# Optimization experiments

Measured on AMD Instinct MI355X. Metric: run time of the kernel, lower is better.

Reference implementation:

```python
import jax, jax.numpy as jnp
import numpy as np
from math import sqrt

H = 16
D_MODEL = 1024
D_K = D_MODEL // H
B, S = 2, 2048


def setup_inputs() -> dict:
    key = jax.random.key(0)
    ks = jax.random.split(key, 12)
    scale = 1.0 / sqrt(D_MODEL)
    inp = {
        "query": jax.random.normal(ks[0], (B, S, D_MODEL), jnp.float32),
        "key": jax.random.normal(ks[1], (B, S, D_MODEL), jnp.float32),
        "value": jax.random.normal(ks[2], (B, S, D_MODEL), jnp.float32),
        # causal mask [B, S, S]; module unsqueezes head dim itself
        "mask": jnp.broadcast_to(jnp.tril(jnp.ones((S, S), jnp.int32)), (B, S, S)),
        "Wq": jax.random.normal(ks[3], (D_MODEL, D_MODEL), jnp.float32) * scale,
        "bq": jnp.zeros((D_MODEL,), jnp.float32),
        "Wk": jax.random.normal(ks[4], (D_MODEL, D_MODEL), jnp.float32) * scale,
        "bk": jnp.zeros((D_MODEL,), jnp.float32),
        "Wv": jax.random.normal(ks[5], (D_MODEL, D_MODEL), jnp.float32) * scale,
        "bv": jnp.zeros((D_MODEL,), jnp.float32),
        "Wo": jax.random.normal(ks[6], (D_MODEL, D_MODEL), jnp.float32) * scale,
        "bo": jnp.zeros((D_MODEL,), jnp.float32),
    }
    return inp


def reference(query, key, value, mask, Wq, bq, Wk, bk, Wv, bv, Wo, bo):
    nb = query.shape[0]

    def proj(x, W, b):
        # nn.Linear: x @ W.T + b, then split heads -> [B, H, S, D_K]
        y = jnp.einsum('bsd,ed->bse', x, W) + b
        return y.reshape(nb, -1, H, D_K).transpose(0, 2, 1, 3)

    q = proj(query, Wq, bq)
    k = proj(key, Wk, bk)
    v = proj(value, Wv, bv)

    scores = jnp.einsum('bhqd,bhkd->bhqk', q, k) / sqrt(D_K)  # [B,H,S,S]
    scores = jnp.where(mask[:, None, :, :] == 0, -jnp.inf, scores)
    probs = jax.nn.softmax(scores, axis=-1)  # dropout in eval mode (identity)
    ctx = jnp.einsum('bhqk,bhkd->bhqd', probs, v)
    ctx = ctx.transpose(0, 2, 1, 3).reshape(nb, -1, H * D_K)
    return jnp.einsum('bsd,ed->bse', ctx, Wo) + bo
```

## Files before the change

### kernel.cpp

```cpp
#include <hip/hip_runtime.h>
#include <hip/hip_bf16.h>
#include <stdint.h>


#define H_ 16
#define DM 1024
#define DK_ 64
#define BB 2
#define SS 2048
#define PSTR 72

typedef __bf16 bf16x8 __attribute__((ext_vector_type(8)));
typedef __bf16 bf16x2_t __attribute__((ext_vector_type(2)));
typedef float f32x4 __attribute__((ext_vector_type(4)));

#define GLOAD_LDS16(g, l)                                            \
  __builtin_amdgcn_global_load_lds(                                  \
      (__attribute__((address_space(1))) void*)(g),                  \
      (__attribute__((address_space(3))) void*)(l), 16, 0, 0)

__device__ __forceinline__ unsigned short f2bf_u(float f) {
  unsigned int u = __float_as_uint(f);
  u += 0x7fffu + ((u >> 16) & 1u);
  return (unsigned short)(u >> 16);
}

__device__ __forceinline__ unsigned int pack_bf16(float a, float b) {
#if __has_builtin(__builtin_amdgcn_cvt_pk_bf16_f32)
  bf16x2_t v = __builtin_amdgcn_cvt_pk_bf16_f32(a, b);
  unsigned int u;
  __builtin_memcpy(&u, &v, 4);
  return u;
#else
  return (unsigned int)f2bf_u(a) | ((unsigned int)f2bf_u(b) << 16);
#endif
}

__device__ __forceinline__ float fexp2(float x) {
#if __has_builtin(__builtin_amdgcn_exp2f)
  return __builtin_amdgcn_exp2f(x);
#else
  return exp2f(x);
#endif
}

struct Cvt {
  const float* s[7];
  unsigned short* d[7];
  int n[7];
};

__global__ __launch_bounds__(256) void convert_kernel(Cvt c) {
  const int y = blockIdx.y;
  const float* __restrict__ src = c.s[y];
  unsigned short* __restrict__ dst = c.d[y];
  const int nv = c.n[y] >> 2;
  for (int i = blockIdx.x * 256 + threadIdx.x; i < nv; i += 1024 * 256) {
    float4 v = *(const float4*)(src + (size_t)i * 4);
    ushort4 o;
    o.x = f2bf_u(v.x); o.y = f2bf_u(v.y); o.z = f2bf_u(v.z); o.w = f2bf_u(v.w);
    *(ushort4*)(dst + (size_t)i * 4) = o;
  }
}

template <int TN>
__device__ __forceinline__ void gemm_dbuf(
    const unsigned short* __restrict__ A, const unsigned short* __restrict__ W,
    unsigned short* As, unsigned short* Bs, int m0, int n0,
    f32x4 (*acc)[TN / 32]) {
  constexpr int FW = TN / 32;
  const int tid = threadIdx.x;
  const int wave = tid >> 6, lane = tid & 63;
  const int lm = lane & 15, quad = lane >> 4;
  const int wm = (wave >> 1) * 64, wn = (wave & 1) * (16 * FW);
  const int srow = lane >> 2;
  const int scol = (lane & 3) * 8;

#pragma unroll
  for (int i = 0; i < 4; ++i)
#pragma unroll
    for (int j = 0; j < FW; ++j) {
      f32x4 z = {0.f, 0.f, 0.f, 0.f};
      acc[i][j] = z;
    }

#pragma unroll
  for (int cc = 0; cc < 2; ++cc) {
    int c = wave * 2 + cc;
    GLOAD_LDS16(A + (size_t)(m0 + c * 16 + srow) * DM + scol,
                As + c * 512 + lane * 8);
  }
  if (TN == 128) {
#pragma unroll
    for (int cc = 0; cc < 2; ++cc) {
      int c = wave * 2 + cc;
      GLOAD_LDS16(W + (size_t)(n0 + c * 16 + srow) * DM + scol,
                  Bs + c * 512 + lane * 8);
    }
  } else {
    GLOAD_LDS16(W + (size_t)(n0 + wave * 16 + srow) * DM + scol,
                Bs + wave * 512 + lane * 8);
  }

  for (int kt = 0; kt < DM / 32; ++kt) {
    __syncthreads();
    const int cur = kt & 1;
    const unsigned short* Ac = As + cur * (128 * 32);
    const unsigned short* Bc = Bs + cur * (TN * 32);
    if (kt + 1 < DM / 32) {
      unsigned short* An = As + (cur ^ 1) * (128 * 32);
      unsigned short* Bn = Bs + (cur ^ 1) * (TN * 32);
      const int kcol = (kt + 1) * 32 + scol;
#pragma unroll
      for (int cc = 0; cc < 2; ++cc) {
        int c = wave * 2 + cc;
        GLOAD_LDS16(A + (size_t)(m0 + c * 16 + srow) * DM + kcol,
                    An + c * 512 + lane * 8);
      }
      if (TN == 128) {
#pragma unroll
        for (int cc = 0; cc < 2; ++cc) {
          int c = wave * 2 + cc;
          GLOAD_LDS16(W + (size_t)(n0 + c * 16 + srow) * DM + kcol,
                      Bn + c * 512 + lane * 8);
        }
      } else {
        GLOAD_LDS16(W + (size_t)(n0 + wave * 16 + srow) * DM + kcol,
                    Bn + wave * 512 + lane * 8);
      }
    }
    bf16x8 af[4], bfr[FW];
#pragma unroll
    for (int i = 0; i < 4; ++i)
      af[i] = *(const bf16x8*)(Ac + (wm + i * 16 + lm) * 32 + quad * 8);
#pragma unroll
    for (int j = 0; j < FW; ++j)
      bfr[j] = *(const bf16x8*)(Bc + (wn + j * 16 + lm) * 32 + quad * 8);
#pragma unroll
    for (int i = 0; i < 4; ++i)
#pragma unroll
      for (int j = 0; j < FW; ++j)
        acc[i][j] = __builtin_amdgcn_mfma_f32_16x16x32_bf16(af[i], bfr[j],
                                                            acc[i][j], 0, 0, 0);
  }
}

__global__ __launch_bounds__(512, 2) void qkv_gemm(
    const unsigned short* Qi, const unsigned short* Ki, const unsigned short* Vi,
    const unsigned short* Wq, const unsigned short* Wk, const unsigned short* Wv,
    const float* bq, const float* bk, const float* bv,
    unsigned short* Qf, unsigned short* Kf, unsigned short* Vf) {
  __shared__ unsigned short As[2 * 2 * 16 * 512];
  __shared__ unsigned short Bs[2 * 2 * 16 * 512];
  const int p = blockIdx.x;
  const int c = p & 7, idx = p >> 3;
  const int x = idx & 3, yy = (idx >> 2) & 1, z = idx >> 3;
  const int y = c * 2 + yy;
  const int m0 = y * 256, n0 = x * 256;
  const unsigned short* A = z == 0 ? Qi : (z == 1 ? Ki : Vi);
  const unsigned short* W = z == 0 ? Wq : (z == 1 ? Wk : Wv);
  const float* bias = z == 0 ? bq : (z == 1 ? bk : bv);
  const float scale = z == 0 ? 0.1803368801111204f : 1.0f;

  const int tid = threadIdx.x;
  const int wave = tid >> 6, lane = tid & 63;
  const int lm = lane & 15, quad = lane >> 4;
  const int wr = wave >> 2, wc = wave & 3;

  const int scs = 8 * ((lane & 3) ^ ((lane >> 3) & 3));
  const size_t asrc0 = (size_t)(m0 + wave * 16 + (lane >> 2)) * DM + scs;
  const size_t bsrc0 = (size_t)(n0 + wave * 16 + (lane >> 2)) * DM + scs;
  const int sdst = wave * 512 + lane * 8;

  const int rcol = (quad * 8) ^ (((lm >> 1) & 3) * 8);
  const int aoff = wr * 8 * 512 + lm * 32 + rcol;
  const int boff = wc * 4 * 512 + lm * 32 + rcol;

  f32x4 acc[8][4];
#pragma unroll
  for (int i = 0; i < 8; ++i)
#pragma unroll
    for (int j = 0; j < 4; ++j) {
      f32x4 zz = {0.f, 0.f, 0.f, 0.f};
      acc[i][j] = zz;
    }

  auto stA = [&](int buf, int kh, int kt) {
    const unsigned short* s = A + asrc0 + (size_t)kt * 64 + kh * 32;
    unsigned short* d = As + buf * 16384 + kh * 8192 + sdst;
    GLOAD_LDS16(s, d);
    GLOAD_LDS16(s + (size_t)128 * DM, d + 4096);
  };
  auto stB = [&](int buf, int kh, int kt) {
    const unsigned short* s = W + bsrc0 + (size_t)kt * 64 + kh * 32;
    unsigned short* d = Bs + buf * 16384 + kh * 8192 + sdst;
    GLOAD_LDS16(s, d);
    GLOAD_LDS16(s + (size_t)128 * DM, d + 4096);
  };

  stA(0, 0, 0); stB(0, 0, 0); stA(0, 1, 0); stB(0, 1, 0);
  stA(1, 0, 1); stB(1, 0, 1); stA(1, 1, 1);
  asm volatile("s_waitcnt vmcnt(6)" ::: "memory");
  __builtin_amdgcn_s_barrier();

#define BARR __builtin_amdgcn_s_barrier()
#define SCHB __builtin_amdgcn_sched_barrier(0)
#define MFMA8(AF, B0_, B1_, J0, J1)                                          \
  __builtin_amdgcn_s_setprio(1);                                             \
  _Pragma("unroll")                                                          \
  for (int i = 0; i < 8; ++i) {                                              \
    acc[i][J0] = __builtin_amdgcn_mfma_f32_16x16x32_bf16(AF[i], B0_,         \
                                                         acc[i][J0], 0, 0, 0); \
    acc[i][J1] = __builtin_amdgcn_mfma_f32_16x16x32_bf16(AF[i], B1_,         \
                                                         acc[i][J1], 0, 0, 0); \
  }                                                                          \
  __builtin_amdgcn_s_setprio(0)

#pragma unroll 2
  for (int t = 0; t < 14; ++t) {
    const int buf = t & 1;
    const unsigned short* Ab = As + buf * 16384;
    const unsigned short* Bb = Bs + buf * 16384;
    bf16x8 a0[8], b0[4];
#pragma unroll
    for (int i = 0; i < 8; ++i)
      a0[i] = *(const bf16x8*)(Ab + aoff + i * 512);
#pragma unroll
    for (int j = 0; j < 4; ++j)
      b0[j] = *(const bf16x8*)(Bb + boff + j * 512);
    stB(buf ^ 1, 1, t + 1);
    BARR; SCHB;
    MFMA8(a0, b0[0], b0[1], 0, 1);
    SCHB; BARR;
    stA(buf, 0, t + 2);
    BARR; SCHB;
    MFMA8(a0, b0[2], b0[3], 2, 3);
    SCHB; BARR;
    bf16x8 a1[8], b1[4];
#pragma unroll
    for (int i = 0; i < 8; ++i)
      a1[i] = *(const bf16x8*)(Ab + 8192 + aoff + i * 512);
#pragma unroll
    for (int j = 0; j < 4; ++j)
      b1[j] = *(const bf16x8*)(Bb + 8192 + boff + j * 512);
    stB(buf, 0, t + 2);
    BARR; SCHB;
    MFMA8(a1, b1[0], b1[1], 0, 1);
    SCHB; BARR;
    stA(buf, 1, t + 2);
    asm volatile("s_waitcnt vmcnt(6)" ::: "memory");
    BARR; SCHB;
    MFMA8(a1, b1[2], b1[3], 2, 3);
    SCHB; BARR;
  }

  stB(1, 1, 15);
  asm volatile("s_waitcnt vmcnt(0)" ::: "memory");
  __builtin_amdgcn_s_barrier();
#pragma unroll
  for (int tt = 0; tt < 2; ++tt) {
    const unsigned short* Ab = As + tt * 16384;
    const unsigned short* Bb = Bs + tt * 16384;
#pragma unroll
    for (int kh = 0; kh < 2; ++kh) {
      bf16x8 a2[8], b2[4];
#pragma unroll
      for (int i = 0; i < 8; ++i)
        a2[i] = *(const bf16x8*)(Ab + kh * 8192 + aoff + i * 512);
#pragma unroll
      for (int j = 0; j < 4; ++j)
        b2[j] = *(const bf16x8*)(Bb + kh * 8192 + boff + j * 512);
#pragma unroll
      for (int i = 0; i < 8; ++i)
#pragma unroll
        for (int j = 0; j < 4; ++j)
          acc[i][j] = __builtin_amdgcn_mfma_f32_16x16x32_bf16(
              a2[i], b2[j], acc[i][j], 0, 0, 0);
    }
  }
#undef MFMA8
#undef SCHB
#undef BARR

  if (z == 2) {
#pragma unroll
    for (int j = 0; j < 4; ++j) {
      int gn = n0 + wc * 64 + j * 16 + lm;
      float bv_ = bias[gn];
      int h2 = gn >> 6, dk = gn & 63;
      int a = dk >> 4, ln = dk & 15;
#pragma unroll
      for (int i = 0; i < 8; ++i) {
        int s0 = m0 + wr * 128 + i * 16 + quad * 4;
        int b2 = s0 >> 11, sl = s0 & 2047;
        int kt2 = sl >> 6, cc2 = (sl >> 5) & 1, qk = (sl >> 3) & 3, j0 = sl & 7;
        size_t base =
            ((size_t)(((b2 * 16 + h2) * 32 + kt2) * 4 + a) * 2 + cc2) * 512 +
            (qk * 16 + ln) * 8 + j0;
        uint2 w;
        w.x = pack_bf16(acc[i][j][0] + bv_, acc[i][j][1] + bv_);
        w.y = pack_bf16(acc[i][j][2] + bv_, acc[i][j][3] + bv_);
        *(uint2*)(Vf + base) = w;
      }
    }
  } else {
    unsigned short* out = z == 0 ? Qf : Kf;
#pragma unroll
    for (int j = 0; j < 4; ++j) {
      int gn = n0 + wc * 64 + j * 16 + lm;
      float bv_ = bias[gn];
      int h2 = gn >> 6, d64 = gn & 63;
      int cc2 = (d64 >> 5) & 1, qk = (d64 >> 3) & 3, jjq = d64 & 7;
#pragma unroll
      for (int i = 0; i < 8; ++i)
#pragma unroll
        for (int r = 0; r < 4; ++r) {
          int gm = m0 + wr * 128 + i * 16 + quad * 4 + r;
          int b2 = gm >> 11, sl = gm & 2047;
          size_t base =
              ((size_t)((b2 * 16 + h2) * 128 + (sl >> 4)) * 2 + cc2) * 512 +
              (qk * 16 + (sl & 15)) * 8 + jjq;
          out[base] = f2bf_u((acc[i][j][r] + bv_) * scale);
        }
    }
  }
}

__global__ __launch_bounds__(256) void o_gemm(
    const unsigned short* Ctx, const unsigned short* Wo, const float* bo,
    float* out) {
  __shared__ unsigned short As[2 * 128 * 32], Bs[2 * 64 * 32];
  const int p = blockIdx.x;
  const int c = p & 7, j0 = p >> 3;
  const int x = j0 & 15, yy = j0 >> 4;
  const int y = c * 4 + yy;
  const int m0 = y * 128, n0 = x * 64;
  f32x4 acc[4][2];
  gemm_dbuf<64>(Ctx, Wo, As, Bs, m0, n0, acc);
  const int lane = threadIdx.x & 63, wave = threadIdx.x >> 6;
  const int lm = lane & 15, quad = lane >> 4;
  const int wm = (wave >> 1) * 64, wn = (wave & 1) * 32;
#pragma unroll
  for (int j = 0; j < 2; ++j) {
    int gn = n0 + wn + j * 16 + lm;
    float bv_ = bo[gn];
#pragma unroll
    for (int i = 0; i < 4; ++i)
#pragma unroll
      for (int r = 0; r < 4; ++r) {
        int gm = m0 + wm + i * 16 + quad * 4 + r;
        out[(size_t)gm * DM + gn] = acc[i][j][r] + bv_;
      }
  }
}

__global__ __launch_bounds__(256, 2) void attn_kernel(
    const unsigned short* __restrict__ Qf, const unsigned short* __restrict__ Kf,
    const unsigned short* __restrict__ Vf, unsigned short* __restrict__ Ctx) {
  __shared__ float Rs[4][64][21];
  __shared__ unsigned short Ps[4][16 * PSTR];
  const int p = blockIdx.x;
  const int bh = p & 31, qt = 31 - (p >> 5);
  const int b = bh >> 4, h = bh & 15;
  const int tid = threadIdx.x, wave = tid >> 6, lane = tid & 63;
  const int lm = lane & 15, quad = lane >> 4;

  const int qbase0 = qt * 64;
  const int nkw = qt + 1;

  const unsigned short* Kb = Kf + (size_t)bh * 256 * 512;
  const unsigned short* Vb = Vf + (size_t)bh * 256 * 512;
  unsigned short* Pw = Ps[wave];

  bf16x8 onesf;
  {
    unsigned short ob[8] = {0x3F80, 0x3F80, 0x3F80, 0x3F80,
                            0x3F80, 0x3F80, 0x3F80, 0x3F80};
    __builtin_memcpy(&onesf, ob, 16);
  }

  bf16x8 qf[4][2];
#pragma unroll
  for (int f = 0; f < 4; ++f)
#pragma unroll
    for (int c = 0; c < 2; ++c)
      qf[f][c] = *(const bf16x8*)(Qf +
          ((size_t)(bh * 128 + qt * 4 + f) * 2 + c) * 512 + lane * 8);

  f32x4 oacc[4][4];
#pragma unroll
  for (int f = 0; f < 4; ++f)
#pragma unroll
    for (int a = 0; a < 4; ++a) {
      f32x4 z = {0.f, 0.f, 0.f, 0.f};
      oacc[f][a] = z;
    }
  f32x4 lacc[4];
#pragma unroll
  for (int f = 0; f < 4; ++f) {
    f32x4 z = {0.f, 0.f, 0.f, 0.f};
    lacc[f] = z;
  }

  for (int kt = wave; kt < nkw; kt += 4) {
    bf16x8 kf[4][2], vf[4][2];
#pragma unroll
    for (int ik = 0; ik < 4; ++ik)
#pragma unroll
      for (int c = 0; c < 2; ++c)
        kf[ik][c] = *(const bf16x8*)(Kb +
            ((size_t)(kt * 4 + ik) * 2 + c) * 512 + lane * 8);
#pragma unroll
    for (int a = 0; a < 4; ++a)
#pragma unroll
      for (int c = 0; c < 2; ++c)
        vf[a][c] = *(const bf16x8*)(Vb +
            ((size_t)(kt * 8 + a * 2 + c)) * 512 + lane * 8);
    const bool last = (kt == nkw - 1);

#pragma unroll
    for (int f = 0; f < 4; ++f) {
      f32x4 s[4];
#pragma unroll
      for (int ik = 0; ik < 4; ++ik) {
        f32x4 zz = {0.f, 0.f, 0.f, 0.f};
        zz = __builtin_amdgcn_mfma_f32_16x16x32_bf16(kf[ik][0], qf[f][0], zz,
                                                     0, 0, 0);
        s[ik] = __builtin_amdgcn_mfma_f32_16x16x32_bf16(kf[ik][1], qf[f][1],
                                                        zz, 0, 0, 0);
      }
      if (last) {
        int qg = qbase0 + f * 16 + lm;
#pragma unroll
        for (int ik = 0; ik < 4; ++ik)
#pragma unroll
          for (int r = 0; r < 4; ++r) {
            int kg = kt * 64 + ik * 16 + quad * 4 + r;
            if (kg > qg) s[ik][r] = -1e30f;
          }
      }
#pragma unroll
      for (int ik = 0; ik < 4; ++ik) {
        float p0 = fexp2(s[ik][0]);
        float p1 = fexp2(s[ik][1]);
        float p2 = fexp2(s[ik][2]);
        float p3 = fexp2(s[ik][3]);
        uint2 w;
        w.x = pack_bf16(p0, p1);
        w.y = pack_bf16(p2, p3);
        *(uint2*)(Pw + lm * PSTR + ik * 16 + quad * 4) = w;
      }
      bf16x8 pf[2];
#pragma unroll
      for (int c = 0; c < 2; ++c)
        pf[c] = *(const bf16x8*)(Pw + lm * PSTR + c * 32 + quad * 8);
#pragma unroll
      for (int a = 0; a < 4; ++a) {
        oacc[f][a] = __builtin_amdgcn_mfma_f32_16x16x32_bf16(pf[0], vf[a][0],
                                                             oacc[f][a], 0, 0, 0);
        oacc[f][a] = __builtin_amdgcn_mfma_f32_16x16x32_bf16(pf[1], vf[a][1],
                                                             oacc[f][a], 0, 0, 0);
      }
      lacc[f] = __builtin_amdgcn_mfma_f32_16x16x32_bf16(pf[0], onesf, lacc[f],
                                                        0, 0, 0);
      lacc[f] = __builtin_amdgcn_mfma_f32_16x16x32_bf16(pf[1], onesf, lacc[f],
                                                        0, 0, 0);
    }
  }

  const size_t obase = (size_t)(b * SS) * DM + (size_t)h * DK_;
#pragma unroll
  for (int f = 0; f < 4; ++f) {
    __syncthreads();
#pragma unroll
    for (int a = 0; a < 4; ++a)
#pragma unroll
      for (int r = 0; r < 4; ++r)
        Rs[wave][lane][a * 4 + r] = oacc[f][a][r];
#pragma unroll
    for (int r = 0; r < 4; ++r)
      Rs[wave][lane][16 + r] = lacc[f][r];
    __syncthreads();
#pragma unroll
    for (int r = 0; r < 4; ++r) {
      float ov = Rs[0][lane][wave * 4 + r] + Rs[1][lane][wave * 4 + r] +
                 Rs[2][lane][wave * 4 + r] + Rs[3][lane][wave * 4 + r];
      float lv = Rs[0][lane][16 + r] + Rs[1][lane][16 + r] +
                 Rs[2][lane][16 + r] + Rs[3][lane][16 + r];
      int qg = qbase0 + f * 16 + quad * 4 + r;
      Ctx[obase + (size_t)qg * DM + wave * 16 + lm] = f2bf_u(ov / lv);
    }
  }
}

extern "C" void kernel_launch(void* const* d_in, const int* in_sizes, int n_in,
                              void* d_out, int out_size, void* d_ws, size_t ws_size,
                              hipStream_t stream) {
  const float* q = (const float*)d_in[0];
  const float* k = (const float*)d_in[1];
  const float* v = (const float*)d_in[2];
  const float* Wq = (const float*)d_in[4];
  const float* bq = (const float*)d_in[5];
  const float* Wk = (const float*)d_in[6];
  const float* bk = (const float*)d_in[7];
  const float* Wv = (const float*)d_in[8];
  const float* bv = (const float*)d_in[9];
  const float* Wo = (const float*)d_in[10];
  const float* bo = (const float*)d_in[11];

  const size_t NX = (size_t)BB * SS * DM;
  const size_t NW = (size_t)DM * DM;
  unsigned short* ws = (unsigned short*)d_ws;
  unsigned short* Qi = ws;
  unsigned short* Ki = Qi + NX;
  unsigned short* Vi = Ki + NX;
  unsigned short* Wqb = Vi + NX;
  unsigned short* Wkb = Wqb + NW;
  unsigned short* Wvb = Wkb + NW;
  unsigned short* Wob = Wvb + NW;
  unsigned short* Qfr = Wob + NW;
  unsigned short* Kfr = Qfr + NX;
  unsigned short* Vfr = Kfr + NX;
  unsigned short* Ctx = Vfr + NX;

  Cvt c;
  c.s[0] = q; c.s[1] = k; c.s[2] = v; c.s[3] = Wq; c.s[4] = Wk; c.s[5] = Wv; c.s[6] = Wo;
  c.d[0] = Qi; c.d[1] = Ki; c.d[2] = Vi; c.d[3] = Wqb; c.d[4] = Wkb; c.d[5] = Wvb; c.d[6] = Wob;
  c.n[0] = c.n[1] = c.n[2] = (int)NX;
  c.n[3] = c.n[4] = c.n[5] = c.n[6] = (int)NW;

  convert_kernel<<<dim3(1024, 7), dim3(256), 0, stream>>>(c);
  qkv_gemm<<<dim3(192), dim3(512), 0, stream>>>(Qi, Ki, Vi, Wqb, Wkb, Wvb,
                                                bq, bk, bv, Qfr, Kfr, Vfr);
  attn_kernel<<<dim3(1024), dim3(256), 0, stream>>>(Qfr, Kfr, Vfr, Ctx);
  o_gemm<<<dim3(512), dim3(256), 0, stream>>>(Ctx, Wob, bo, (float*)d_out);
}
```

Measured before the change: 228.3 us.

## Swizzle LDS in O-projection GEMM with BK=64 and prefetch K tiles in attention

The O-projection GEMM gets its own inlined main loop. It uses a 64-wide K step split into two 32-wide halves, with an XOR swizzle on both the LDS writes and the fragment reads to avoid bank conflicts, and only half as many barriers. In the attention kernel, K fragments for the next key tile are loaded into a second register set before the current tile is computed, so global load latency overlaps with the MFMA work. The cost is higher register pressure in the attention kernel and more LDS-index arithmetic in the GEMM.

```diff
diff --git a/kernel.cpp b/kernel.cpp
--- a/kernel.cpp
+++ b/kernel.cpp
@@ -60,88 +60,6 @@
     ushort4 o;
     o.x = f2bf_u(v.x); o.y = f2bf_u(v.y); o.z = f2bf_u(v.z); o.w = f2bf_u(v.w);
     *(ushort4*)(dst + (size_t)i * 4) = o;
-  }
-}
-
-template <int TN>
-__device__ __forceinline__ void gemm_dbuf(
-    const unsigned short* __restrict__ A, const unsigned short* __restrict__ W,
-    unsigned short* As, unsigned short* Bs, int m0, int n0,
-    f32x4 (*acc)[TN / 32]) {
-  constexpr int FW = TN / 32;
-  const int tid = threadIdx.x;
-  const int wave = tid >> 6, lane = tid & 63;
-  const int lm = lane & 15, quad = lane >> 4;
-  const int wm = (wave >> 1) * 64, wn = (wave & 1) * (16 * FW);
-  const int srow = lane >> 2;
-  const int scol = (lane & 3) * 8;
-
-#pragma unroll
-  for (int i = 0; i < 4; ++i)
-#pragma unroll
-    for (int j = 0; j < FW; ++j) {
-      f32x4 z = {0.f, 0.f, 0.f, 0.f};
-      acc[i][j] = z;
-    }
-
-#pragma unroll
-  for (int cc = 0; cc < 2; ++cc) {
-    int c = wave * 2 + cc;
-    GLOAD_LDS16(A + (size_t)(m0 + c * 16 + srow) * DM + scol,
-                As + c * 512 + lane * 8);
-  }
-  if (TN == 128) {
-#pragma unroll
-    for (int cc = 0; cc < 2; ++cc) {
-      int c = wave * 2 + cc;
-      GLOAD_LDS16(W + (size_t)(n0 + c * 16 + srow) * DM + scol,
-                  Bs + c * 512 + lane * 8);
-    }
-  } else {
-    GLOAD_LDS16(W + (size_t)(n0 + wave * 16 + srow) * DM + scol,
-                Bs + wave * 512 + lane * 8);
-  }
-
-  for (int kt = 0; kt < DM / 32; ++kt) {
-    __syncthreads();
-    const int cur = kt & 1;
-    const unsigned short* Ac = As + cur * (128 * 32);
-    const unsigned short* Bc = Bs + cur * (TN * 32);
-    if (kt + 1 < DM / 32) {
-      unsigned short* An = As + (cur ^ 1) * (128 * 32);
-      unsigned short* Bn = Bs + (cur ^ 1) * (TN * 32);
-      const int kcol = (kt + 1) * 32 + scol;
-#pragma unroll
-      for (int cc = 0; cc < 2; ++cc) {
-        int c = wave * 2 + cc;
-        GLOAD_LDS16(A + (size_t)(m0 + c * 16 + srow) * DM + kcol,
-                    An + c * 512 + lane * 8);
-      }
-      if (TN == 128) {
-#pragma unroll
-        for (int cc = 0; cc < 2; ++cc) {
-          int c = wave * 2 + cc;
-          GLOAD_LDS16(W + (size_t)(n0 + c * 16 + srow) * DM + kcol,
-                      Bn + c * 512 + lane * 8);
-        }
-      } else {
-        GLOAD_LDS16(W + (size_t)(n0 + wave * 16 + srow) * DM + kcol,
-                    Bn + wave * 512 + lane * 8);
-      }
-    }
-    bf16x8 af[4], bfr[FW];
-#pragma unroll
-    for (int i = 0; i < 4; ++i)
-      af[i] = *(const bf16x8*)(Ac + (wm + i * 16 + lm) * 32 + quad * 8);
-#pragma unroll
-    for (int j = 0; j < FW; ++j)
-      bfr[j] = *(const bf16x8*)(Bc + (wn + j * 16 + lm) * 32 + quad * 8);
-#pragma unroll
-    for (int i = 0; i < 4; ++i)
-#pragma unroll
-      for (int j = 0; j < FW; ++j)
-        acc[i][j] = __builtin_amdgcn_mfma_f32_16x16x32_bf16(af[i], bfr[j],
-                                                            acc[i][j], 0, 0, 0);
   }
 }
 
@@ -329,17 +247,75 @@
 __global__ __launch_bounds__(256) void o_gemm(
     const unsigned short* Ctx, const unsigned short* Wo, const float* bo,
     float* out) {
-  __shared__ unsigned short As[2 * 128 * 32], Bs[2 * 64 * 32];
+  __shared__ unsigned short As[2 * 2 * 8 * 512];
+  __shared__ unsigned short Bs[2 * 2 * 4 * 512];
   const int p = blockIdx.x;
   const int c = p & 7, j0 = p >> 3;
   const int x = j0 & 15, yy = j0 >> 4;
   const int y = c * 4 + yy;
   const int m0 = y * 128, n0 = x * 64;
-  f32x4 acc[4][2];
-  gemm_dbuf<64>(Ctx, Wo, As, Bs, m0, n0, acc);
-  const int lane = threadIdx.x & 63, wave = threadIdx.x >> 6;
+  const int tid = threadIdx.x;
+  const int wave = tid >> 6, lane = tid & 63;
   const int lm = lane & 15, quad = lane >> 4;
   const int wm = (wave >> 1) * 64, wn = (wave & 1) * 32;
+
+  const int scs = 8 * ((lane & 3) ^ ((lane >> 3) & 3));
+  const int srow = lane >> 2;
+  const size_t aSrc0 = (size_t)(m0 + wave * 32 + srow) * DM + scs;
+  const size_t bSrc0 = (size_t)(n0 + wave * 16 + srow) * DM + scs;
+  const int aDst0 = wave * 2 * 512 + lane * 8;
+  const int bDst0 = wave * 512 + lane * 8;
+
+  const int rcol = (quad * 8) ^ (((lm >> 1) & 3) * 8);
+  const int aoff = (wm >> 4) * 512 + lm * 32 + rcol;
+  const int boff = (wn >> 4) * 512 + lm * 32 + rcol;
+
+  f32x4 acc[4][2];
+#pragma unroll
+  for (int i = 0; i < 4; ++i)
+#pragma unroll
+    for (int j = 0; j < 2; ++j) {
+      f32x4 z = {0.f, 0.f, 0.f, 0.f};
+      acc[i][j] = z;
+    }
+
+  auto stAB = [&](int buf, int kt) {
+#pragma unroll
+    for (int kh = 0; kh < 2; ++kh) {
+      const unsigned short* sa = Ctx + aSrc0 + (size_t)kt * 64 + kh * 32;
+      unsigned short* da = As + buf * 8192 + kh * 4096 + aDst0;
+      GLOAD_LDS16(sa, da);
+      GLOAD_LDS16(sa + (size_t)16 * DM, da + 512);
+      const unsigned short* sb = Wo + bSrc0 + (size_t)kt * 64 + kh * 32;
+      GLOAD_LDS16(sb, Bs + buf * 4096 + kh * 2048 + bDst0);
+    }
+  };
+
+  stAB(0, 0);
+  for (int kt = 0; kt < DM / 64; ++kt) {
+    __syncthreads();
+    const int buf = kt & 1;
+    if (kt + 1 < DM / 64) stAB(buf ^ 1, kt + 1);
+    const unsigned short* Ac = As + buf * 8192;
+    const unsigned short* Bc = Bs + buf * 4096;
+#pragma unroll
+    for (int kh = 0; kh < 2; ++kh) {
+      bf16x8 af[4], bf_[2];
+#pragma unroll
+      for (int i = 0; i < 4; ++i)
+        af[i] = *(const bf16x8*)(Ac + kh * 4096 + aoff + i * 512);
+#pragma unroll
+      for (int j = 0; j < 2; ++j)
+        bf_[j] = *(const bf16x8*)(Bc + kh * 2048 + boff + j * 512);
+#pragma unroll
+      for (int i = 0; i < 4; ++i)
+#pragma unroll
+        for (int j = 0; j < 2; ++j)
+          acc[i][j] = __builtin_amdgcn_mfma_f32_16x16x32_bf16(
+              af[i], bf_[j], acc[i][j], 0, 0, 0);
+    }
+  }
+
 #pragma unroll
   for (int j = 0; j < 2; ++j) {
     int gn = n0 + wn + j * 16 + lm;
@@ -402,21 +378,23 @@
     lacc[f] = z;
   }
 
-  for (int kt = wave; kt < nkw; kt += 4) {
-    bf16x8 kf[4][2], vf[4][2];
+  auto loadK = [&](bf16x8 (&kf)[4][2], int kt) {
 #pragma unroll
     for (int ik = 0; ik < 4; ++ik)
 #pragma unroll
       for (int c = 0; c < 2; ++c)
         kf[ik][c] = *(const bf16x8*)(Kb +
             ((size_t)(kt * 4 + ik) * 2 + c) * 512 + lane * 8);
+  };
+
+  auto computeKt = [&](bf16x8 (&kf)[4][2], int kt, bool last) {
+    bf16x8 vf[4][2];
 #pragma unroll
     for (int a = 0; a < 4; ++a)
 #pragma unroll
       for (int c = 0; c < 2; ++c)
         vf[a][c] = *(const bf16x8*)(Vb +
             ((size_t)(kt * 8 + a * 2 + c)) * 512 + lane * 8);
-    const bool last = (kt == nkw - 1);
 
 #pragma unroll
     for (int f = 0; f < 4; ++f) {
@@ -465,6 +443,17 @@
                                                         0, 0, 0);
       lacc[f] = __builtin_amdgcn_mfma_f32_16x16x32_bf16(pf[1], onesf, lacc[f],
                                                         0, 0, 0);
+    }
+  };
+
+  bf16x8 kA[4][2], kB[4][2];
+  if (wave < nkw) loadK(kA, wave);
+  for (int kt = wave; kt < nkw; kt += 8) {
+    if (kt + 4 < nkw) loadK(kB, kt + 4);
+    computeKt(kA, kt, kt == nkw - 1);
+    if (kt + 4 < nkw) {
+      if (kt + 8 < nkw) loadK(kA, kt + 8);
+      computeKt(kB, kt + 4, kt + 4 == nkw - 1);
     }
   }
 
```

After: 226.9 us. Within noise of the previous version (-0.6%).
